# Optimization experiments

Measured on AMD Instinct MI355X. Metric: run time of the kernel, lower is better.

Reference implementation:

```python
import jax, jax.numpy as jnp
import numpy as np

ALPHA = 2.0   # spikingjelly surrogate.ATan default
TAU = 2.0     # LIFNode default
VTH = 1.0     # v_threshold
T = 16

@jax.custom_vjp
def atan_spike(u):
    # heaviside forward, ATan surrogate backward
    return (u >= 0).astype(u.dtype)

def _atan_fwd(u):
    return atan_spike(u), u

def _atan_bwd(u, g):
    return (g * (ALPHA / 2.0) / (1.0 + (jnp.pi / 2.0 * ALPHA * u) ** 2),)

atan_spike.defvjp(_atan_fwd, _atan_bwd)


def setup_inputs() -> dict:
    key = jax.random.key(0)
    ks = jax.random.split(key, 7)
    n_in, n_hid, n_out, B = 512, 1024, 6, 16384

    def lin(k, fan_in, shape):
        bound = 1.0 / np.sqrt(fan_in)
        return jax.random.uniform(k, shape, jnp.float32, -bound, bound)

    return {
        "x": jax.random.normal(ks[0], (B, n_in), jnp.float32),
        "W1": lin(ks[1], n_in, (n_hid, n_in)),
        "b1": lin(ks[2], n_in, (n_hid,)),
        "W2": lin(ks[3], n_hid, (n_hid, n_hid)),
        "b2": lin(ks[4], n_hid, (n_hid,)),
        "W3": lin(ks[5], n_hid, (n_out, n_hid)),
        "b3": lin(ks[6], n_hid, (n_out,)),
    }


def reference(x, W1, b1, W2, b2, W3, b3):
    # Input is static across timesteps -> fc1 output is loop-invariant.
    i1 = x @ W1.T + b1  # [B, n_hid]
    B = x.shape[0]
    init = (
        jnp.zeros((B, W1.shape[0]), x.dtype),  # v1
        jnp.zeros((B, W2.shape[0]), x.dtype),  # v2
        jnp.zeros((B, W3.shape[0]), x.dtype),  # v3
    )

    def lif(v, i):
        # charge: v += (i - (v - v_reset)) / tau, v_reset = 0
        v = v + (i - v) / TAU
        s = atan_spike(v - VTH)
        # hard reset to v_reset = 0 (detach_reset=False -> keep grad path)
        v = v * (1.0 - s)
        return v, s

    def step(carry, _):
        v1, v2, v3 = carry
        v1, s1 = lif(v1, i1)
        v2, s2 = lif(v2, s1 @ W2.T + b2)
        v3, s3 = lif(v3, s2 @ W3.T + b3)
        return (v1, v2, v3), s3

    _, spikes = jax.lax.scan(step, init, None, length=T)  # [T, B, n_out]
    return spikes.sum(axis=0) / T
```

## Files before the change

kernel.cpp:

```cpp
#include <hip/hip_runtime.h>
#include <hip/hip_bf16.h>


typedef _Float16 f16;
typedef __attribute__((ext_vector_type(4))) _Float16 f16x4;
typedef __attribute__((ext_vector_type(8))) _Float16 f16x8;
typedef __attribute__((ext_vector_type(4))) float f32x4;

__global__ __launch_bounds__(256) void k_cvt(const float* __restrict__ x,
                                             const float* __restrict__ W1,
                                             f16* __restrict__ xh,
                                             f16* __restrict__ W1h) {
    const int NX = 16384 * 512 / 4;
    const int NW = 1024 * 512 / 4;
    int i = blockIdx.x * 256 + threadIdx.x;
    const int stride = gridDim.x * 256;
    for (; i < NX + NW; i += stride) {
        const float4* src;
        f16* dst;
        int j;
        if (i < NX) { src = (const float4*)x; dst = xh; j = i; }
        else        { src = (const float4*)W1; dst = W1h; j = i - NX; }
        float4 v = src[j];
        f16x4 h;
        h.x = (f16)v.x; h.y = (f16)v.y; h.z = (f16)v.z; h.w = (f16)v.w;
        *(f16x4*)(dst + (size_t)4 * j) = h;
    }
}

__global__ void k_tq(const float* __restrict__ W2, unsigned char* __restrict__ W2u) {
    __shared__ float t[32][33];
    const int bj = blockIdx.x;
    const int bk = blockIdx.y;
    const int tx = threadIdx.x;
    const int ty = threadIdx.y;
#pragma unroll
    for (int i = 0; i < 32; i += 8)
        t[ty + i][tx] = W2[(size_t)(bj * 32 + ty + i) * 1024 + bk * 32 + tx];
    __syncthreads();
#pragma unroll
    for (int i = 0; i < 32; i += 8) {
        float v = t[tx][ty + i];
        int q = (int)rintf(v * 4064.0f);
        q = q > 127 ? 127 : (q < -127 ? -127 : q);
        W2u[(size_t)(bk * 32 + ty + i) * 1024 + bj * 32 + tx] = (unsigned char)(q + 128);
    }
}

__global__ __launch_bounds__(256) void k_fc1(const f16* __restrict__ xh,
                                             const f16* __restrict__ W1h,
                                             const float* __restrict__ b1,
                                             f16* __restrict__ i1h) {
    __shared__ __align__(16) f16 Atile[128 * 32];
    __shared__ __align__(16) f16 Btile[256 * 32];
    const int tid = threadIdx.x;
    const int lane = tid & 63;
    const int wid = tid >> 6;
    const int wm = wid >> 1;
    const int wn = wid & 1;
    const int m0 = blockIdx.x * 128;
    const int n0 = blockIdx.y * 256;

    f32x4 acc[4][8] = {};

    for (int k0 = 0; k0 < 512; k0 += 32) {
        __syncthreads();
#pragma unroll
        for (int q = 0; q < 6; ++q) {
            const bool isA = (q < 2);
            int u = q * 256 + tid;
            int cu = isA ? u : (u - 512);
            int rl = cu >> 2;
            int slot = (cu & 3) ^ (rl & 3);
            const f16* g = isA
                ? xh  + (size_t)(m0 + rl) * 512 + k0 + slot * 8
                : W1h + (size_t)(n0 + rl) * 512 + k0 + slot * 8;
            f16x8 v = *(const f16x8*)g;
            f16* d = (isA ? Atile : Btile) + (size_t)cu * 8;
            *(f16x8*)d = v;
        }
        __syncthreads();
        f16x8 af[4], bf[8];
#pragma unroll
        for (int i = 0; i < 4; ++i) {
            int rowA = (wm << 6) + (i << 4) + (lane & 15);
            af[i] = *(const f16x8*)(Atile + rowA * 32 + (((lane >> 4) ^ (rowA & 3)) << 3));
        }
#pragma unroll
        for (int j = 0; j < 8; ++j) {
            int rowB = (wn << 7) + (j << 4) + (lane & 15);
            bf[j] = *(const f16x8*)(Btile + rowB * 32 + (((lane >> 4) ^ (rowB & 3)) << 3));
        }
#pragma unroll
        for (int i = 0; i < 4; ++i)
#pragma unroll
            for (int j = 0; j < 8; ++j)
                acc[i][j] = __builtin_amdgcn_mfma_f32_16x16x32_f16(af[i], bf[j], acc[i][j], 0, 0, 0);
    }

    float b1v[8];
#pragma unroll
    for (int j = 0; j < 8; ++j)
        b1v[j] = b1[n0 + (wn << 7) + (j << 4) + (lane & 15)];
#pragma unroll
    for (int i = 0; i < 4; ++i) {
        int rm = m0 + (wm << 6) + (i << 4) + ((lane >> 4) << 2);
#pragma unroll
        for (int j = 0; j < 8; ++j) {
            int cn = n0 + (wn << 7) + (j << 4) + (lane & 15);
            f16* op = i1h + (size_t)rm * 1024 + cn;
#pragma unroll
            for (int rr = 0; rr < 4; ++rr)
                op[(size_t)rr * 1024] = (f16)(acc[i][j][rr] + b1v[j]);
        }
    }
}

__global__ __launch_bounds__(256) void k_snn(const f16* __restrict__ i1g,
                                             const unsigned char* __restrict__ W2u,
                                             const float* __restrict__ b2,
                                             const float* __restrict__ W3,
                                             const float* __restrict__ b3,
                                             float* __restrict__ out) {
    const int lane = threadIdx.x & 63;
    const int wid = threadIdx.x >> 6;
    const int r = blockIdx.x * 4 + wid;
    const float DEQ = 1.0f / 4064.0f;

    unsigned train[16];
    unsigned cnt[8] = {};
    const f16x4* i1p4 = (const f16x4*)(i1g + (size_t)r * 1024);
#pragma unroll
    for (int g = 0; g < 4; ++g) {
        f16x4 tq = i1p4[lane + 64 * g];
#pragma unroll
        for (int e = 0; e < 4; ++e) {
            float iv = (float)tq[e];
            float v = 0.0f;
            unsigned tr = 0u;
#pragma unroll
            for (int t = 0; t < 16; ++t) {
                v = v + (iv - v) * 0.5f;
                unsigned su = (v >= 1.0f) ? 1u : 0u;
                v = su ? 0.0f : v;
                tr |= su << t;
                cnt[t >> 1] += su << ((t & 1) * 16);
            }
            train[4 * g + e] = tr;
        }
    }
#pragma unroll
    for (int st = 1; st < 64; st <<= 1)
#pragma unroll
        for (int h = 0; h < 8; ++h)
            cnt[h] += __shfl_xor(cnt[h], st, 64);

    float b2r[16];
#pragma unroll
    for (int q = 0; q < 4; ++q) {
        float4 u = ((const float4*)b2)[lane * 4 + q];
        b2r[4 * q + 0] = u.x; b2r[4 * q + 1] = u.y;
        b2r[4 * q + 2] = u.z; b2r[4 * q + 3] = u.w;
    }
    float b3r[6];
#pragma unroll
    for (int m6 = 0; m6 < 6; ++m6) b3r[m6] = b3[m6];

    const uint4* w2v = (const uint4*)W2u;

    float v2[16] = {}, v3[6] = {}, cnt3[6] = {};

#pragma unroll
    for (int half = 0; half < 2; ++half) {
        unsigned accE[8][4] = {};
        unsigned accO[8][4] = {};
#pragma unroll
        for (int g = 0; g < 4; ++g)
#pragma unroll
            for (int e = 0; e < 4; ++e) {
                unsigned sub = (train[4 * g + e] >> (half * 8)) & 0xFFu;
                unsigned long long m = __ballot(sub != 0u);
                if (m) {
                    int b0 = __builtin_ctzll(m); m &= m - 1;
                    unsigned tr0 = __builtin_amdgcn_readlane(sub, b0);
                    uint4 w0 = w2v[(size_t)(4 * b0 + 256 * g + e) * 64 + lane];
                    while (m) {
                        int b1 = __builtin_ctzll(m); m &= m - 1;
                        unsigned tr1 = __builtin_amdgcn_readlane(sub, b1);
                        uint4 w1 = w2v[(size_t)(4 * b1 + 256 * g + e) * 64 + lane];
                        {
                            unsigned E[4], O[4];
                            E[0] = __builtin_amdgcn_perm(0u, w0.x, 0x04020400u);
                            O[0] = __builtin_amdgcn_perm(0u, w0.x, 0x04030401u);
                            E[1] = __builtin_amdgcn_perm(0u, w0.y, 0x04020400u);
                            O[1] = __builtin_amdgcn_perm(0u, w0.y, 0x04030401u);
                            E[2] = __builtin_amdgcn_perm(0u, w0.z, 0x04020400u);
                            O[2] = __builtin_amdgcn_perm(0u, w0.z, 0x04030401u);
                            E[3] = __builtin_amdgcn_perm(0u, w0.w, 0x04020400u);
                            O[3] = __builtin_amdgcn_perm(0u, w0.w, 0x04030401u);
#pragma unroll
                            for (int tt = 0; tt < 8; ++tt)
                                if (tr0 & (1u << tt)) {
#pragma unroll
                                    for (int d = 0; d < 4; ++d) {
                                        accE[tt][d] += E[d];
                                        accO[tt][d] += O[d];
                                    }
                                }
                        }
                        tr0 = tr1; w0 = w1;
                    }
                    {
                        unsigned E[4], O[4];
                        E[0] = __builtin_amdgcn_perm(0u, w0.x, 0x04020400u);
                        O[0] = __builtin_amdgcn_perm(0u, w0.x, 0x04030401u);
                        E[1] = __builtin_amdgcn_perm(0u, w0.y, 0x04020400u);
                        O[1] = __builtin_amdgcn_perm(0u, w0.y, 0x04030401u);
                        E[2] = __builtin_amdgcn_perm(0u, w0.z, 0x04020400u);
                        O[2] = __builtin_amdgcn_perm(0u, w0.z, 0x04030401u);
                        E[3] = __builtin_amdgcn_perm(0u, w0.w, 0x04020400u);
                        O[3] = __builtin_amdgcn_perm(0u, w0.w, 0x04030401u);
#pragma unroll
                        for (int tt = 0; tt < 8; ++tt)
                            if (tr0 & (1u << tt)) {
#pragma unroll
                                for (int d = 0; d < 4; ++d) {
                                    accE[tt][d] += E[d];
                                    accO[tt][d] += O[d];
                                }
                            }
                    }
                }
            }
#pragma unroll
        for (int tt = 0; tt < 8; ++tt) {
            const int t = half * 8 + tt;
            const int nr = (int)((cnt[t >> 1] >> ((t & 1) * 16)) & 0xFFFFu);
            const int bias = nr << 7;
            bool s2[16];
#pragma unroll
            for (int d = 0; d < 4; ++d) {
                int sq[4];
                sq[0] = (int)(accE[tt][d] & 0xFFFFu) - bias;
                sq[1] = (int)(accO[tt][d] & 0xFFFFu) - bias;
                sq[2] = (int)(accE[tt][d] >> 16) - bias;
                sq[3] = (int)(accO[tt][d] >> 16) - bias;
#pragma unroll
                for (int c = 0; c < 4; ++c) {
                    int e = 4 * d + c;
                    float i2 = fmaf((float)sq[c], DEQ, b2r[e]);
                    float v = v2[e];
                    v = v + (i2 - v) * 0.5f;
                    bool s = v >= 1.0f;
                    s2[e] = s;
                    v2[e] = s ? 0.0f : v;
                }
            }
            float i3[6];
#pragma unroll
            for (int m6 = 0; m6 < 6; ++m6) i3[m6] = b3r[m6];
#pragma unroll
            for (int e = 0; e < 16; ++e) {
                unsigned long long mm = __ballot(s2[e] ? 1 : 0);
                while (mm) {
                    int b = __builtin_ctzll(mm);
                    mm &= mm - 1;
                    int j = 16 * b + e;
#pragma unroll
                    for (int m6 = 0; m6 < 6; ++m6) i3[m6] += W3[m6 * 1024 + j];
                }
            }
#pragma unroll
            for (int m6 = 0; m6 < 6; ++m6) {
                float v = v3[m6];
                v = v + (i3[m6] - v) * 0.5f;
                bool s = v >= 1.0f;
                cnt3[m6] += s ? 1.0f : 0.0f;
                v3[m6] = s ? 0.0f : v;
            }
        }
    }
    if (lane == 0) {
#pragma unroll
        for (int m6 = 0; m6 < 6; ++m6)
            out[(size_t)r * 6 + m6] = cnt3[m6] * 0.0625f;
    }
}

extern "C" void kernel_launch(void* const* d_in, const int* in_sizes, int n_in,
                              void* d_out, int out_size, void* d_ws, size_t ws_size,
                              hipStream_t stream) {
    const float* x  = (const float*)d_in[0];
    const float* W1 = (const float*)d_in[1];
    const float* b1 = (const float*)d_in[2];
    const float* W2 = (const float*)d_in[3];
    const float* b2 = (const float*)d_in[4];
    const float* W3 = (const float*)d_in[5];
    const float* b3 = (const float*)d_in[6];
    float* out = (float*)d_out;

    char* ws = (char*)d_ws;
    f16* i1h = (f16*)ws;
    f16* xh  = (f16*)(ws + ((size_t)32 << 20));
    f16* W1h = (f16*)(ws + ((size_t)48 << 20));
    unsigned char* W2u = (unsigned char*)(ws + ((size_t)49 << 20));

    k_cvt<<<2048, 256, 0, stream>>>(x, W1, xh, W1h);
    k_tq<<<dim3(32, 32), dim3(32, 8), 0, stream>>>(W2, W2u);
    k_fc1<<<dim3(128, 4), 256, 0, stream>>>(xh, W1h, b1, i1h);
    k_snn<<<4096, 256, 0, stream>>>(i1h, W2u, b2, W3, b3, out);
}
```

Baseline: 380.6 us.

## Compact active spike rows into LDS list and prefetch W2 rows four ahead

Instead of walking ballot masks per (g,e) group with a one-deep prefetch, each wave first compacts all active input neurons and their 8-step spike trains into a shared-memory list. It then streams W2 rows through a 4-deep double-buffered register pipeline, giving more loads in flight. It also skips the per-element W3 ballot loop when no layer-2 neuron in the wave spiked. The cost is extra LDS traffic, more registers for the prefetch buffers, and list padding that loads a few dummy rows.

Result: slower. 432.8 us (+13.7%).

```diff
diff --git a/kernel.cpp b/kernel.cpp
--- a/kernel.cpp
+++ b/kernel.cpp
@@ -122,6 +122,7 @@
                                              const float* __restrict__ W3,
                                              const float* __restrict__ b3,
                                              float* __restrict__ out) {
+    __shared__ unsigned lst[4][272];
     const int lane = threadIdx.x & 63;
     const int wid = threadIdx.x >> 6;
     const int r = blockIdx.x * 4 + wid;
@@ -172,8 +173,7 @@
 
 #pragma unroll
     for (int half = 0; half < 2; ++half) {
-        unsigned accE[8][4] = {};
-        unsigned accO[8][4] = {};
+        int n = 0;
 #pragma unroll
         for (int g = 0; g < 4; ++g)
 #pragma unroll
@@ -181,63 +181,68 @@
                 unsigned sub = (train[4 * g + e] >> (half * 8)) & 0xFFu;
                 unsigned long long m = __ballot(sub != 0u);
                 if (m) {
-                    int b0 = __builtin_ctzll(m); m &= m - 1;
-                    unsigned tr0 = __builtin_amdgcn_readlane(sub, b0);
-                    uint4 w0 = w2v[(size_t)(4 * b0 + 256 * g + e) * 64 + lane];
-                    while (m) {
-                        int b1 = __builtin_ctzll(m); m &= m - 1;
-                        unsigned tr1 = __builtin_amdgcn_readlane(sub, b1);
-                        uint4 w1 = w2v[(size_t)(4 * b1 + 256 * g + e) * 64 + lane];
-                        {
-                            unsigned E[4], O[4];
-                            E[0] = __builtin_amdgcn_perm(0u, w0.x, 0x04020400u);
-                            O[0] = __builtin_amdgcn_perm(0u, w0.x, 0x04030401u);
-                            E[1] = __builtin_amdgcn_perm(0u, w0.y, 0x04020400u);
-                            O[1] = __builtin_amdgcn_perm(0u, w0.y, 0x04030401u);
-                            E[2] = __builtin_amdgcn_perm(0u, w0.z, 0x04020400u);
-                            O[2] = __builtin_amdgcn_perm(0u, w0.z, 0x04030401u);
-                            E[3] = __builtin_amdgcn_perm(0u, w0.w, 0x04020400u);
-                            O[3] = __builtin_amdgcn_perm(0u, w0.w, 0x04030401u);
-#pragma unroll
-                            for (int tt = 0; tt < 8; ++tt)
-                                if (tr0 & (1u << tt)) {
-#pragma unroll
-                                    for (int d = 0; d < 4; ++d) {
-                                        accE[tt][d] += E[d];
-                                        accO[tt][d] += O[d];
-                                    }
-                                }
+                    int idx = (int)__popcll(m & ((1ull << lane) - 1ull));
+                    if (sub)
+                        lst[wid][n + idx] =
+                            (unsigned)(4 * lane + 256 * g + e) | (sub << 16);
+                    n += (int)__popcll(m);
+                }
+            }
+        if (lane < 8) lst[wid][n + lane] = 0u;
+
+        unsigned accE[8][4] = {};
+        unsigned accO[8][4] = {};
+
+        if (n) {
+            unsigned enA[4];
+            uint4 wA[4];
+#pragma unroll
+            for (int u = 0; u < 4; ++u) {
+                enA[u] = lst[wid][u];
+                wA[u] = w2v[(size_t)(enA[u] & 0xFFFFu) * 64 + lane];
+            }
+            for (int i = 0; i < n; i += 4) {
+                unsigned enB[4];
+                uint4 wB[4];
+#pragma unroll
+                for (int u = 0; u < 4; ++u) {
+                    enB[u] = lst[wid][i + 4 + u];
+                    wB[u] = w2v[(size_t)(enB[u] & 0xFFFFu) * 64 + lane];
+                }
+#pragma unroll
+                for (int u = 0; u < 4; ++u) {
+                    unsigned tr = __builtin_amdgcn_readfirstlane(enA[u]) >> 16;
+                    unsigned E[4], O[4];
+                    E[0] = __builtin_amdgcn_perm(0u, wA[u].x, 0x04020400u);
+                    O[0] = __builtin_amdgcn_perm(0u, wA[u].x, 0x04030401u);
+                    E[1] = __builtin_amdgcn_perm(0u, wA[u].y, 0x04020400u);
+                    O[1] = __builtin_amdgcn_perm(0u, wA[u].y, 0x04030401u);
+                    E[2] = __builtin_amdgcn_perm(0u, wA[u].z, 0x04020400u);
+                    O[2] = __builtin_amdgcn_perm(0u, wA[u].z, 0x04030401u);
+                    E[3] = __builtin_amdgcn_perm(0u, wA[u].w, 0x04020400u);
+                    O[3] = __builtin_amdgcn_perm(0u, wA[u].w, 0x04030401u);
+#pragma unroll
+                    for (int tt = 0; tt < 8; ++tt)
+                        if (tr & (1u << tt)) {
+#pragma unroll
+                            for (int d = 0; d < 4; ++d) {
+                                accE[tt][d] += E[d];
+                                accO[tt][d] += O[d];
+                            }
                         }
-                        tr0 = tr1; w0 = w1;
-                    }
-                    {
-                        unsigned E[4], O[4];
-                        E[0] = __builtin_amdgcn_perm(0u, w0.x, 0x04020400u);
-                        O[0] = __builtin_amdgcn_perm(0u, w0.x, 0x04030401u);
-                        E[1] = __builtin_amdgcn_perm(0u, w0.y, 0x04020400u);
-                        O[1] = __builtin_amdgcn_perm(0u, w0.y, 0x04030401u);
-                        E[2] = __builtin_amdgcn_perm(0u, w0.z, 0x04020400u);
-                        O[2] = __builtin_amdgcn_perm(0u, w0.z, 0x04030401u);
-                        E[3] = __builtin_amdgcn_perm(0u, w0.w, 0x04020400u);
-                        O[3] = __builtin_amdgcn_perm(0u, w0.w, 0x04030401u);
-#pragma unroll
-                        for (int tt = 0; tt < 8; ++tt)
-                            if (tr0 & (1u << tt)) {
-#pragma unroll
-                                for (int d = 0; d < 4; ++d) {
-                                    accE[tt][d] += E[d];
-                                    accO[tt][d] += O[d];
-                                }
-                            }
-                    }
-                }
-            }
+                }
+#pragma unroll
+                for (int u = 0; u < 4; ++u) { enA[u] = enB[u]; wA[u] = wB[u]; }
+            }
+        }
+
 #pragma unroll
         for (int tt = 0; tt < 8; ++tt) {
             const int t = half * 8 + tt;
             const int nr = (int)((cnt[t >> 1] >> ((t & 1) * 16)) & 0xFFFFu);
             const int bias = nr << 7;
             bool s2[16];
+            bool any2 = false;
 #pragma unroll
             for (int d = 0; d < 4; ++d) {
                 int sq[4];
@@ -253,21 +258,24 @@
                     v = v + (i2 - v) * 0.5f;
                     bool s = v >= 1.0f;
                     s2[e] = s;
+                    any2 |= s;
                     v2[e] = s ? 0.0f : v;
                 }
             }
             float i3[6];
 #pragma unroll
             for (int m6 = 0; m6 < 6; ++m6) i3[m6] = b3r[m6];
-#pragma unroll
-            for (int e = 0; e < 16; ++e) {
-                unsigned long long mm = __ballot(s2[e] ? 1 : 0);
-                while (mm) {
-                    int b = __builtin_ctzll(mm);
-                    mm &= mm - 1;
-                    int j = 16 * b + e;
-#pragma unroll
-                    for (int m6 = 0; m6 < 6; ++m6) i3[m6] += W3[m6 * 1024 + j];
+            if (__ballot(any2 ? 1 : 0)) {
+#pragma unroll
+                for (int e = 0; e < 16; ++e) {
+                    unsigned long long mm = __ballot(s2[e] ? 1 : 0);
+                    while (mm) {
+                        int b = __builtin_ctzll(mm);
+                        mm &= mm - 1;
+                        int j = 16 * b + e;
+#pragma unroll
+                        for (int m6 = 0; m6 < 6; ++m6) i3[m6] += W3[m6 * 1024 + j];
+                    }
                 }
             }
 #pragma unroll
```
